# Kernel optimization log

Measured on AMD Instinct MI355X. Metric: run time of the kernel, lower is better.

Reference implementation:

```python
import jax, jax.numpy as jnp
import numpy as np

N_NODES = 100000
N_EDGES = 500000
IN_DIM, HID, N_CLS = 128, 512, 40


def gcn_conv(x, W, b, src, dst, num_nodes):
    # PyG GCNConv: h = x W; add self-loops; norm = d^-1/2[src] * d^-1/2[dst];
    # out[dst] += norm * h[src]; out += bias
    h = x @ W  # [N, out_dim]
    ones = jnp.ones(src.shape[0], dtype=x.dtype)
    deg = jax.ops.segment_sum(ones, dst, num_segments=num_nodes)  # in-degree incl self-loops
    dinv = jnp.where(deg > 0, jax.lax.rsqrt(deg), 0.0)
    norm = dinv[src] * dinv[dst]  # [E]
    msgs = h[src] * norm[:, None]  # [E, out_dim] gather + scale
    out = jax.ops.segment_sum(msgs, dst, num_segments=num_nodes)
    return out + b


def setup_inputs() -> dict:
    key = jax.random.key(0)
    k1, k2, k3, k4, k5, k6 = jax.random.split(key, 6)
    x = jax.random.normal(k1, (N_NODES, IN_DIM), dtype=jnp.float32)
    edge_index = jax.random.randint(k2, (2, N_EDGES), 0, N_NODES, dtype=jnp.int32)
    # Glorot-ish params
    W1 = jax.random.normal(k3, (IN_DIM, HID), dtype=jnp.float32) * (1.0 / np.sqrt(IN_DIM))
    b1 = jnp.zeros((HID,), dtype=jnp.float32)
    W2 = jax.random.normal(k4, (HID, N_CLS), dtype=jnp.float32) * (1.0 / np.sqrt(HID))
    b2 = jnp.zeros((N_CLS,), dtype=jnp.float32)
    return {"x": x, "edge_index": edge_index, "W1": W1, "b1": b1, "W2": W2, "b2": b2}


def reference(x, edge_index, W1, b1, W2, b2):
    n = x.shape[0]
    # add self-loops once, shared by both conv layers
    loop = jnp.arange(n, dtype=edge_index.dtype)
    src = jnp.concatenate([edge_index[0], loop])
    dst = jnp.concatenate([edge_index[1], loop])
    h = gcn_conv(x, W1, b1, src, dst, n)
    h = jax.nn.relu(h)
    # dropout is identity in eval mode (reference computed in eval)
    h = gcn_conv(h, W2, b2, src, dst, n)
    return jax.nn.log_softmax(h, axis=1)
```

## Files before the change

kernel.cpp:

```cpp
#include <hip/hip_runtime.h>
#include <cstdint>
#include <cstddef>

#define N_NODES 100000
#define N_EDGES 500000
#define IN_DIM  128
#define HID     512
#define N_CLS   40
#define N_SBLK  ((N_NODES + 255) / 256)
#define N_CNTB  ((N_EDGES + 255) / 256)
#define N_XBFB  12500
#define N_PREPB 352

typedef short bf16x8 __attribute__((ext_vector_type(8)));
typedef float f32x4 __attribute__((ext_vector_type(4)));

__device__ inline unsigned short f2bf(float f) {
  unsigned u = __float_as_uint(f);
  u = u + 0x7fffu + ((u >> 16) & 1u);
  return (unsigned short)(u >> 16);
}
__device__ inline float blo(unsigned u) { return __uint_as_float(u << 16); }
__device__ inline float bhi(unsigned u) { return __uint_as_float(u & 0xffff0000u); }
__device__ inline float bf2f(unsigned short s) { return __uint_as_float((unsigned)s << 16); }

__global__ __launch_bounds__(256) void k_zero(int* __restrict__ cnt) {
  int i = blockIdx.x * 256 + threadIdx.x;
  if (i < N_NODES) cnt[i] = 0;
}

__global__ __launch_bounds__(256) void k_count_xbf(const int* __restrict__ dst, int* __restrict__ cnt,
                                                   const float* __restrict__ x, uint2* __restrict__ xb2) {
  int b = blockIdx.x;
  if (b < N_CNTB) {
    int e = b * 256 + threadIdx.x;
    if (e < N_EDGES) atomicAdd(&cnt[dst[e]], 1);
  } else {
    int t = (b - N_CNTB) * 256 + threadIdx.x;
    float4 v = ((const float4*)x)[t];
    uint2 o;
    o.x = (unsigned)f2bf(v.x) | ((unsigned)f2bf(v.y) << 16);
    o.y = (unsigned)f2bf(v.z) | ((unsigned)f2bf(v.w) << 16);
    xb2[t] = o;
  }
}

__global__ __launch_bounds__(256) void k_scan1(const int* __restrict__ cnt, int* __restrict__ lofs,
                                               int* __restrict__ blksum, float* __restrict__ dinv) {
  __shared__ int s[256];
  int i = blockIdx.x * 256 + threadIdx.x;
  int v = (i < N_NODES) ? cnt[i] : 0;
  s[threadIdx.x] = v;
  __syncthreads();
  #pragma unroll
  for (int off = 1; off < 256; off <<= 1) {
    int t = (threadIdx.x >= off) ? s[threadIdx.x - off] : 0;
    __syncthreads();
    s[threadIdx.x] += t;
    __syncthreads();
  }
  if (i < N_NODES) {
    lofs[i] = s[threadIdx.x] - v;
    dinv[i] = rsqrtf((float)(v + 1));
  }
  if (threadIdx.x == 255) blksum[blockIdx.x] = s[255];
}

__global__ __launch_bounds__(512) void k_scan2(const int* __restrict__ blksum, int* __restrict__ blkbase) {
  __shared__ int s[512];
  int t = threadIdx.x;
  int v = (t < N_SBLK) ? blksum[t] : 0;
  s[t] = v;
  __syncthreads();
  #pragma unroll
  for (int off = 1; off < 512; off <<= 1) {
    int u = (t >= off) ? s[t - off] : 0;
    __syncthreads();
    s[t] += u;
    __syncthreads();
  }
  if (t < N_SBLK) blkbase[t] = s[t] - v;
}

__global__ __launch_bounds__(256) void k_scan3_prep(const int* __restrict__ lofs, const int* __restrict__ blkbase,
                                                    int* __restrict__ offsets, int* __restrict__ cursor,
                                                    const float* __restrict__ W1, const float* __restrict__ W2,
                                                    unsigned short* __restrict__ W1F, unsigned short* __restrict__ W2F) {
  int b = blockIdx.x;
  if (b < N_SBLK) {
    int i = b * 256 + threadIdx.x;
    if (b == 0 && threadIdx.x == 0) offsets[N_NODES] = N_EDGES;
    if (i >= N_NODES) return;
    int base = blkbase[b] + lofs[i];
    offsets[i] = base;
    cursor[i]  = base;
  } else {
    int t = (b - N_SBLK) * 256 + threadIdx.x;
    if (t < 65536) {
      int j = t & 7, lane = (t >> 3) & 63, rest = t >> 9;
      int s = rest & 3, c = rest >> 2;
      int k = s * 32 + (lane >> 4) * 8 + j;
      int n = c * 16 + (lane & 15);
      W1F[t] = f2bf(W1[k * HID + n]);
    } else {
      int u = t - 65536;
      int j = u & 7, lane = (u >> 3) & 63, rest = u >> 9;
      int ct = rest % 3, gk = rest / 3;
      int k = gk * 32 + (lane >> 4) * 8 + j;
      int col = ct * 16 + (lane & 15);
      W2F[u] = (col < N_CLS) ? f2bf(W2[k * N_CLS + col]) : (unsigned short)0;
    }
  }
}

__global__ __launch_bounds__(256) void k_fill(const int* __restrict__ src, const int* __restrict__ dst,
                                              const float* __restrict__ dinv,
                                              int* __restrict__ cursor, int2* __restrict__ epair) {
  int e = blockIdx.x * 256 + threadIdx.x;
  if (e >= N_EDGES) return;
  int s = src[e], d = dst[e];
  int pos = atomicAdd(&cursor[d], 1);
  float nrm = dinv[s] * dinv[d];
  epair[pos] = make_int2(s, __float_as_int(nrm));
}

__global__ __launch_bounds__(256) void k_gather1(const uint4* __restrict__ xb4, const int2* __restrict__ ep,
                                                 const int* __restrict__ offsets,
                                                 const float* __restrict__ dinv, uint4* __restrict__ z1b4) {
  int d = blockIdx.x * 4 + (threadIdx.x >> 6);
  if (d >= N_NODES) return;
  int lane = threadIdx.x & 63, q = lane >> 4, l16 = lane & 15;
  int start = offsets[d], end = offsets[d + 1];

  float a0 = 0.f, a1 = 0.f, a2 = 0.f, a3 = 0.f, a4 = 0.f, a5 = 0.f, a6 = 0.f, a7 = 0.f;
  if (q == 0) {
    float dd = dinv[d], sl = dd * dd;
    uint4 u = xb4[(size_t)d * 16 + l16];
    a0 = sl * blo(u.x); a1 = sl * bhi(u.x); a2 = sl * blo(u.y); a3 = sl * bhi(u.y);
    a4 = sl * blo(u.z); a5 = sl * bhi(u.z); a6 = sl * blo(u.w); a7 = sl * bhi(u.w);
  }

  int i = start + q;
  for (; i + 4 < end; i += 8) {
    int2 p0 = ep[i], p1 = ep[i + 4];
    uint4 r0 = xb4[(size_t)p0.x * 16 + l16];
    uint4 r1 = xb4[(size_t)p1.x * 16 + l16];
    float n0 = __int_as_float(p0.y), n1 = __int_as_float(p1.y);
    a0 += n0 * blo(r0.x); a1 += n0 * bhi(r0.x); a2 += n0 * blo(r0.y); a3 += n0 * bhi(r0.y);
    a4 += n0 * blo(r0.z); a5 += n0 * bhi(r0.z); a6 += n0 * blo(r0.w); a7 += n0 * bhi(r0.w);
    a0 += n1 * blo(r1.x); a1 += n1 * bhi(r1.x); a2 += n1 * blo(r1.y); a3 += n1 * bhi(r1.y);
    a4 += n1 * blo(r1.z); a5 += n1 * bhi(r1.z); a6 += n1 * blo(r1.w); a7 += n1 * bhi(r1.w);
  }
  for (; i < end; i += 4) {
    int2 p = ep[i];
    uint4 r = xb4[(size_t)p.x * 16 + l16];
    float n = __int_as_float(p.y);
    a0 += n * blo(r.x); a1 += n * bhi(r.x); a2 += n * blo(r.y); a3 += n * bhi(r.y);
    a4 += n * blo(r.z); a5 += n * bhi(r.z); a6 += n * blo(r.w); a7 += n * bhi(r.w);
  }

  a0 += __shfl_xor(a0, 16, 64); a0 += __shfl_xor(a0, 32, 64);
  a1 += __shfl_xor(a1, 16, 64); a1 += __shfl_xor(a1, 32, 64);
  a2 += __shfl_xor(a2, 16, 64); a2 += __shfl_xor(a2, 32, 64);
  a3 += __shfl_xor(a3, 16, 64); a3 += __shfl_xor(a3, 32, 64);
  a4 += __shfl_xor(a4, 16, 64); a4 += __shfl_xor(a4, 32, 64);
  a5 += __shfl_xor(a5, 16, 64); a5 += __shfl_xor(a5, 32, 64);
  a6 += __shfl_xor(a6, 16, 64); a6 += __shfl_xor(a6, 32, 64);
  a7 += __shfl_xor(a7, 16, 64); a7 += __shfl_xor(a7, 32, 64);
  if (q == 0) {
    uint4 o;
    o.x = (unsigned)f2bf(a0) | ((unsigned)f2bf(a1) << 16);
    o.y = (unsigned)f2bf(a2) | ((unsigned)f2bf(a3) << 16);
    o.z = (unsigned)f2bf(a4) | ((unsigned)f2bf(a5) << 16);
    o.w = (unsigned)f2bf(a6) | ((unsigned)f2bf(a7) << 16);
    z1b4[(size_t)d * 16 + l16] = o;
  }
}

#define HS_STRIDE 56
__global__ __launch_bounds__(256) void k_fused_mfma(const unsigned short* __restrict__ z1b,
                                                    const unsigned short* __restrict__ W1F,
                                                    const float* __restrict__ b1,
                                                    const unsigned short* __restrict__ W2F,
                                                    unsigned short* __restrict__ Pb) {
  __shared__ unsigned short Hs[4][64 * HS_STRIDE];
  const int tid  = threadIdx.x;
  const int w    = tid >> 6, lane = tid & 63;
  const int c16  = lane & 15, quad = lane >> 4;
  const int mbase = blockIdx.x * 256 + w * 64;

  bf16x8 afrag[4][4];
  #pragma unroll
  for (int t = 0; t < 4; ++t) {
    int mrow = mbase + t * 16 + c16;
    int meff = (mrow < N_NODES) ? mrow : 0;
    const bf16x8* arow = (const bf16x8*)(z1b + (size_t)meff * IN_DIM + quad * 8);
    afrag[t][0] = arow[0];
    afrag[t][1] = arow[4];
    afrag[t][2] = arow[8];
    afrag[t][3] = arow[12];
  }

  f32x4 pacc[4][3];
  #pragma unroll
  for (int t = 0; t < 4; ++t)
    #pragma unroll
    for (int ct = 0; ct < 3; ++ct) pacc[t][ct] = (f32x4){0.f, 0.f, 0.f, 0.f};

  const bf16x8* w1f = (const bf16x8*)W1F;
  const bf16x8* w2f = (const bf16x8*)W2F;
  unsigned short* hs = Hs[w];

  for (int g = 0; g < 16; ++g) {
    #pragma unroll
    for (int nt = 0; nt < 2; ++nt) {
      int c = g * 2 + nt;
      bf16x8 bp0 = w1f[(c * 4 + 0) * 64 + lane];
      bf16x8 bp1 = w1f[(c * 4 + 1) * 64 + lane];
      bf16x8 bp2 = w1f[(c * 4 + 2) * 64 + lane];
      bf16x8 bp3 = w1f[(c * 4 + 3) * 64 + lane];
      f32x4 h[4];
      #pragma unroll
      for (int t = 0; t < 4; ++t) h[t] = (f32x4){0.f, 0.f, 0.f, 0.f};
      #pragma unroll
      for (int t = 0; t < 4; ++t) h[t] = __builtin_amdgcn_mfma_f32_16x16x32_bf16(afrag[t][0], bp0, h[t], 0, 0, 0);
      #pragma unroll
      for (int t = 0; t < 4; ++t) h[t] = __builtin_amdgcn_mfma_f32_16x16x32_bf16(afrag[t][1], bp1, h[t], 0, 0, 0);
      #pragma unroll
      for (int t = 0; t < 4; ++t) h[t] = __builtin_amdgcn_mfma_f32_16x16x32_bf16(afrag[t][2], bp2, h[t], 0, 0, 0);
      #pragma unroll
      for (int t = 0; t < 4; ++t) h[t] = __builtin_amdgcn_mfma_f32_16x16x32_bf16(afrag[t][3], bp3, h[t], 0, 0, 0);
      float bias = b1[c * 16 + c16];
      #pragma unroll
      for (int t = 0; t < 4; ++t)
        #pragma unroll
        for (int r = 0; r < 4; ++r)
          hs[(t * 16 + quad * 4 + r) * HS_STRIDE + nt * 16 + c16] = f2bf(fmaxf(h[t][r] + bias, 0.f));
    }
    bf16x8 hf[4];
    #pragma unroll
    for (int t = 0; t < 4; ++t)
      hf[t] = *(const bf16x8*)(hs + (t * 16 + c16) * HS_STRIDE + quad * 8);
    #pragma unroll
    for (int ct = 0; ct < 3; ++ct) {
      bf16x8 bf = w2f[(g * 3 + ct) * 64 + lane];
      #pragma unroll
      for (int t = 0; t < 4; ++t)
        pacc[t][ct] = __builtin_amdgcn_mfma_f32_16x16x32_bf16(hf[t], bf, pacc[t][ct], 0, 0, 0);
    }
  }

  #pragma unroll
  for (int t = 0; t < 4; ++t) {
    int mrow0 = mbase + t * 16 + quad * 4;
    #pragma unroll
    for (int ct = 0; ct < 3; ++ct) {
      int col = ct * 16 + c16;
      if (col < N_CLS) {
        #pragma unroll
        for (int r = 0; r < 4; ++r) {
          int m = mrow0 + r;
          if (m < N_NODES) Pb[(size_t)m * N_CLS + col] = f2bf(pacc[t][ct][r]);
        }
      }
    }
  }
}

__global__ __launch_bounds__(256) void k_gather2_lsm(const unsigned* __restrict__ Pu,
                                                     const int2* __restrict__ ep,
                                                     const int* __restrict__ offsets,
                                                     const float* __restrict__ dinv, const float* __restrict__ b2,
                                                     float* __restrict__ out) {
  int lane = threadIdx.x & 63, h = lane >> 5, l32 = lane & 31;
  int d = blockIdx.x * 8 + (threadIdx.x >> 6) * 2 + h;
  bool act = l32 < 20;
  int lc = act ? l32 : 0;
  int start = offsets[d], end = offsets[d + 1];
  float dd = dinv[d];

  float x0, y0, x1 = 0.f, y1 = 0.f, x2 = 0.f, y2 = 0.f, x3 = 0.f, y3 = 0.f;
  {
    unsigned u = Pu[(size_t)d * 20 + lc];
    float sl = dd * dd;
    x0 = sl * blo(u); y0 = sl * bhi(u);
  }
  int i = start;
  for (; i + 3 < end; i += 4) {
    int2 p0 = ep[i], p1 = ep[i + 1], p2 = ep[i + 2], p3 = ep[i + 3];
    unsigned u0 = Pu[(size_t)p0.x * 20 + lc];
    unsigned u1 = Pu[(size_t)p1.x * 20 + lc];
    unsigned u2 = Pu[(size_t)p2.x * 20 + lc];
    unsigned u3 = Pu[(size_t)p3.x * 20 + lc];
    float n0 = __int_as_float(p0.y), n1 = __int_as_float(p1.y);
    float n2 = __int_as_float(p2.y), n3 = __int_as_float(p3.y);
    x0 += n0 * blo(u0); y0 += n0 * bhi(u0);
    x1 += n1 * blo(u1); y1 += n1 * bhi(u1);
    x2 += n2 * blo(u2); y2 += n2 * bhi(u2);
    x3 += n3 * blo(u3); y3 += n3 * bhi(u3);
  }
  for (; i < end; ++i) {
    int2 p = ep[i];
    unsigned u = Pu[(size_t)p.x * 20 + lc];
    float n = __int_as_float(p.y);
    x0 += n * blo(u); y0 += n * bhi(u);
  }

  float v0, v1;
  if (act) {
    float2 bb = *(const float2*)(b2 + 2 * l32);
    v0 = x0 + x1 + x2 + x3 + bb.x;
    v1 = y0 + y1 + y2 + y3 + bb.y;
  } else {
    v0 = v1 = -1e30f;
  }
  float m = fmaxf(v0, v1);
  #pragma unroll
  for (int off = 16; off > 0; off >>= 1) m = fmaxf(m, __shfl_xor(m, off, 64));
  float e = act ? (expf(v0 - m) + expf(v1 - m)) : 0.f;
  float s = e;
  #pragma unroll
  for (int off = 16; off > 0; off >>= 1) s += __shfl_xor(s, off, 64);
  float lse = m + logf(s);
  if (act) {
    float2 o = make_float2(v0 - lse, v1 - lse);
    *(float2*)(out + (size_t)d * N_CLS + 2 * l32) = o;
  }
}

extern "C" void kernel_launch(void* const* d_in, const int* in_sizes, int n_in,
                              void* d_out, int out_size, void* d_ws, size_t ws_size,
                              hipStream_t stream) {
  const float* x  = (const float*)d_in[0];
  const int*   ei = (const int*)d_in[1];
  const int*  src = ei;
  const int*  dst = ei + N_EDGES;
  const float* W1 = (const float*)d_in[2];
  const float* b1 = (const float*)d_in[3];
  const float* W2 = (const float*)d_in[4];
  const float* b2 = (const float*)d_in[5];
  float* out = (float*)d_out;

  float* dinv    = (float*)d_ws;
  int*   cnt     = (int*)(dinv + 131072);
  int*   offsets = cnt + 131072;
  int*   cursor  = offsets + 131072;
  int*   lofs    = cursor + 131072;
  int*   blksum  = lofs + 131072;
  int*   blkbase = blksum + 512;
  int2*  epair   = (int2*)(blkbase + 512);
  uint2* xb2     = (uint2*)(epair + 524288);
  unsigned short* Pb = (unsigned short*)xb2;
  unsigned short* z1b = (unsigned short*)(xb2 + 3200000);
  unsigned short* W1F = z1b + (size_t)N_NODES * IN_DIM;
  unsigned short* W2F = W1F + HID * IN_DIM;

  k_zero <<<(N_NODES + 255) / 256, 256, 0, stream>>>(cnt);
  k_count_xbf<<<N_CNTB + N_XBFB, 256, 0, stream>>>(dst, cnt, x, xb2);
  k_scan1<<<N_SBLK, 256, 0, stream>>>(cnt, lofs, blksum, dinv);
  k_scan2<<<1, 512, 0, stream>>>(blksum, blkbase);
  k_scan3_prep<<<N_SBLK + N_PREPB, 256, 0, stream>>>(lofs, blkbase, offsets, cursor, W1, W2, W1F, W2F);
  k_fill <<<N_CNTB, 256, 0, stream>>>(src, dst, dinv, cursor, epair);
  k_gather1<<<(N_NODES + 3) / 4, 256, 0, stream>>>((const uint4*)xb2, epair, offsets, dinv, (uint4*)z1b);
  k_fused_mfma<<<(N_NODES + 255) / 256, 256, 0, stream>>>(z1b, W1F, b1, W2F, Pb);
  k_gather2_lsm<<<N_NODES / 8, 256, 0, stream>>>((const unsigned*)Pb, epair, offsets, dinv, b2, out);
}
```

Before: 249.2 us.

## Fuse three-pass scan into decoupled look-back scan and remap gather lanes

Replaces the three scan kernels with a single kernel that uses a decoupled look-back (per-block flag/aggregate) prefix scan, cutting two launches and the intermediate arrays. The look-back relies on blocks making forward progress, since a block spins on its predecessor. It also remaps gather1 so each half-wave handles one node with 4 bf16 per lane and four independent accumulators, replacing the quarter-wave split and cross-lane shuffle reduction. Gather2 now packs four nodes per wave with 4 classes per lane.

Measured after the change: 247.4 us. Within noise of the previous version (-0.7%).

```diff
diff --git a/kernel.cpp b/kernel.cpp
--- a/kernel.cpp
+++ b/kernel.cpp
@@ -22,11 +22,11 @@
 }
 __device__ inline float blo(unsigned u) { return __uint_as_float(u << 16); }
 __device__ inline float bhi(unsigned u) { return __uint_as_float(u & 0xffff0000u); }
-__device__ inline float bf2f(unsigned short s) { return __uint_as_float((unsigned)s << 16); }
-
-__global__ __launch_bounds__(256) void k_zero(int* __restrict__ cnt) {
+
+__global__ __launch_bounds__(256) void k_zero(int* __restrict__ cnt, unsigned* __restrict__ flags) {
   int i = blockIdx.x * 256 + threadIdx.x;
   if (i < N_NODES) cnt[i] = 0;
+  if (i < 512) flags[i] = 0;
 }
 
 __global__ __launch_bounds__(256) void k_count_xbf(const int* __restrict__ dst, int* __restrict__ cnt,
@@ -45,61 +45,61 @@
   }
 }
 
-__global__ __launch_bounds__(256) void k_scan1(const int* __restrict__ cnt, int* __restrict__ lofs,
-                                               int* __restrict__ blksum, float* __restrict__ dinv) {
-  __shared__ int s[256];
-  int i = blockIdx.x * 256 + threadIdx.x;
-  int v = (i < N_NODES) ? cnt[i] : 0;
-  s[threadIdx.x] = v;
-  __syncthreads();
-  #pragma unroll
-  for (int off = 1; off < 256; off <<= 1) {
-    int t = (threadIdx.x >= off) ? s[threadIdx.x - off] : 0;
-    __syncthreads();
-    s[threadIdx.x] += t;
-    __syncthreads();
-  }
-  if (i < N_NODES) {
-    lofs[i] = s[threadIdx.x] - v;
-    dinv[i] = rsqrtf((float)(v + 1));
-  }
-  if (threadIdx.x == 255) blksum[blockIdx.x] = s[255];
-}
-
-__global__ __launch_bounds__(512) void k_scan2(const int* __restrict__ blksum, int* __restrict__ blkbase) {
-  __shared__ int s[512];
-  int t = threadIdx.x;
-  int v = (t < N_SBLK) ? blksum[t] : 0;
-  s[t] = v;
-  __syncthreads();
-  #pragma unroll
-  for (int off = 1; off < 512; off <<= 1) {
-    int u = (t >= off) ? s[t - off] : 0;
-    __syncthreads();
-    s[t] += u;
-    __syncthreads();
-  }
-  if (t < N_SBLK) blkbase[t] = s[t] - v;
-}
-
-__global__ __launch_bounds__(256) void k_scan3_prep(const int* __restrict__ lofs, const int* __restrict__ blkbase,
-                                                    int* __restrict__ offsets, int* __restrict__ cursor,
-                                                    const float* __restrict__ W1, const float* __restrict__ W2,
-                                                    unsigned short* __restrict__ W1F, unsigned short* __restrict__ W2F) {
+__global__ __launch_bounds__(256) void k_scan_prep(const int* __restrict__ cnt, unsigned* __restrict__ flags,
+                                                   int* __restrict__ offsets, int* __restrict__ cursor,
+                                                   float* __restrict__ dinv,
+                                                   const float* __restrict__ W1, const float* __restrict__ W2,
+                                                   unsigned short* __restrict__ W1F, unsigned short* __restrict__ W2F) {
   int b = blockIdx.x;
   if (b < N_SBLK) {
+    __shared__ int s[256];
+    __shared__ int base_sh;
     int i = b * 256 + threadIdx.x;
+    int v = (i < N_NODES) ? cnt[i] : 0;
+    s[threadIdx.x] = v;
+    __syncthreads();
+    #pragma unroll
+    for (int off = 1; off < 256; off <<= 1) {
+      int t = (threadIdx.x >= off) ? s[threadIdx.x - off] : 0;
+      __syncthreads();
+      s[threadIdx.x] += t;
+      __syncthreads();
+    }
+    int incl = s[threadIdx.x];
+    if (threadIdx.x == 0) {
+      int total = s[255];
+      if (b == 0) {
+        atomicExch(&flags[0], (2u << 30) | (unsigned)total);
+        base_sh = 0;
+      } else {
+        atomicExch(&flags[b], (1u << 30) | (unsigned)total);
+        int base = 0, pred = b - 1;
+        while (true) {
+          unsigned f;
+          do { f = atomicAdd(&flags[pred], 0u); } while ((f >> 30) == 0u);
+          base += (int)(f & 0x3fffffffu);
+          if ((f >> 30) == 2u) break;
+          --pred;
+        }
+        atomicExch(&flags[b], (2u << 30) | (unsigned)(base + (unsigned)total));
+        base_sh = base;
+      }
+    }
+    __syncthreads();
+    int gbase = base_sh;
+    if (i < N_NODES) {
+      int excl = gbase + incl - v;
+      offsets[i] = excl;
+      cursor[i]  = excl;
+      dinv[i]    = rsqrtf((float)(v + 1));
+    }
     if (b == 0 && threadIdx.x == 0) offsets[N_NODES] = N_EDGES;
-    if (i >= N_NODES) return;
-    int base = blkbase[b] + lofs[i];
-    offsets[i] = base;
-    cursor[i]  = base;
   } else {
     int t = (b - N_SBLK) * 256 + threadIdx.x;
     if (t < 65536) {
       int j = t & 7, lane = (t >> 3) & 63, rest = t >> 9;
-      int s = rest & 3, c = rest >> 2;
-      int k = s * 32 + (lane >> 4) * 8 + j;
+      int s2 = rest & 3, c = rest >> 2;
+      int k = s2 * 32 + (lane >> 4) * 8 + j;
       int n = c * 16 + (lane & 15);
       W1F[t] = f2bf(W1[k * HID + n]);
     } else {
@@ -124,57 +124,47 @@
   epair[pos] = make_int2(s, __float_as_int(nrm));
 }
 
-__global__ __launch_bounds__(256) void k_gather1(const uint4* __restrict__ xb4, const int2* __restrict__ ep,
+__global__ __launch_bounds__(256) void k_gather1(const uint2* __restrict__ xb, const int2* __restrict__ ep,
                                                  const int* __restrict__ offsets,
-                                                 const float* __restrict__ dinv, uint4* __restrict__ z1b4) {
-  int d = blockIdx.x * 4 + (threadIdx.x >> 6);
-  if (d >= N_NODES) return;
-  int lane = threadIdx.x & 63, q = lane >> 4, l16 = lane & 15;
+                                                 const float* __restrict__ dinv, uint2* __restrict__ z1) {
+  int lane = threadIdx.x & 63, h = lane >> 5, l = lane & 31;
+  int d = blockIdx.x * 8 + (threadIdx.x >> 6) * 2 + h;
   int start = offsets[d], end = offsets[d + 1];
-
-  float a0 = 0.f, a1 = 0.f, a2 = 0.f, a3 = 0.f, a4 = 0.f, a5 = 0.f, a6 = 0.f, a7 = 0.f;
-  if (q == 0) {
-    float dd = dinv[d], sl = dd * dd;
-    uint4 u = xb4[(size_t)d * 16 + l16];
-    a0 = sl * blo(u.x); a1 = sl * bhi(u.x); a2 = sl * blo(u.y); a3 = sl * bhi(u.y);
-    a4 = sl * blo(u.z); a5 = sl * bhi(u.z); a6 = sl * blo(u.w); a7 = sl * bhi(u.w);
-  }
-
-  int i = start + q;
-  for (; i + 4 < end; i += 8) {
-    int2 p0 = ep[i], p1 = ep[i + 4];
-    uint4 r0 = xb4[(size_t)p0.x * 16 + l16];
-    uint4 r1 = xb4[(size_t)p1.x * 16 + l16];
-    float n0 = __int_as_float(p0.y), n1 = __int_as_float(p1.y);
+  float dd = dinv[d], sl = dd * dd;
+  uint2 su = xb[(size_t)d * 32 + l];
+  float a0 = sl * blo(su.x), a1 = sl * bhi(su.x), a2 = sl * blo(su.y), a3 = sl * bhi(su.y);
+  float p0a = 0.f, p1a = 0.f, p2a = 0.f, p3a = 0.f;
+  float q0a = 0.f, q1a = 0.f, q2a = 0.f, q3a = 0.f;
+  float r0a = 0.f, r1a = 0.f, r2a = 0.f, r3a = 0.f;
+
+  int i = start;
+  for (; i + 3 < end; i += 4) {
+    int2 e0 = ep[i], e1 = ep[i + 1], e2 = ep[i + 2], e3 = ep[i + 3];
+    uint2 r0 = xb[(size_t)e0.x * 32 + l];
+    uint2 r1 = xb[(size_t)e1.x * 32 + l];
+    uint2 r2 = xb[(size_t)e2.x * 32 + l];
+    uint2 r3 = xb[(size_t)e3.x * 32 + l];
+    float n0 = __int_as_float(e0.y), n1 = __int_as_float(e1.y);
+    float n2 = __int_as_float(e2.y), n3 = __int_as_float(e3.y);
+    a0  += n0 * blo(r0.x); a1  += n0 * bhi(r0.x); a2  += n0 * blo(r0.y); a3  += n0 * bhi(r0.y);
+    p0a += n1 * blo(r1.x); p1a += n1 * bhi(r1.x); p2a += n1 * blo(r1.y); p3a += n1 * bhi(r1.y);
+    q0a += n2 * blo(r2.x); q1a += n2 * bhi(r2.x); q2a += n2 * blo(r2.y); q3a += n2 * bhi(r2.y);
+    r0a += n3 * blo(r3.x); r1a += n3 * bhi(r3.x); r2a += n3 * blo(r3.y); r3a += n3 * bhi(r3.y);
+  }
+  for (; i < end; ++i) {
+    int2 e0 = ep[i];
+    uint2 r0 = xb[(size_t)e0.x * 32 + l];
+    float n0 = __int_as_float(e0.y);
     a0 += n0 * blo(r0.x); a1 += n0 * bhi(r0.x); a2 += n0 * blo(r0.y); a3 += n0 * bhi(r0.y);
-    a4 += n0 * blo(r0.z); a5 += n0 * bhi(r0.z); a6 += n0 * blo(r0.w); a7 += n0 * bhi(r0.w);
-    a0 += n1 * blo(r1.x); a1 += n1 * bhi(r1.x); a2 += n1 * blo(r1.y); a3 += n1 * bhi(r1.y);
-    a4 += n1 * blo(r1.z); a5 += n1 * bhi(r1.z); a6 += n1 * blo(r1.w); a7 += n1 * bhi(r1.w);
-  }
-  for (; i < end; i += 4) {
-    int2 p = ep[i];
-    uint4 r = xb4[(size_t)p.x * 16 + l16];
-    float n = __int_as_float(p.y);
-    a0 += n * blo(r.x); a1 += n * bhi(r.x); a2 += n * blo(r.y); a3 += n * bhi(r.y);
-    a4 += n * blo(r.z); a5 += n * bhi(r.z); a6 += n * blo(r.w); a7 += n * bhi(r.w);
-  }
-
-  a0 += __shfl_xor(a0, 16, 64); a0 += __shfl_xor(a0, 32, 64);
-  a1 += __shfl_xor(a1, 16, 64); a1 += __shfl_xor(a1, 32, 64);
-  a2 += __shfl_xor(a2, 16, 64); a2 += __shfl_xor(a2, 32, 64);
-  a3 += __shfl_xor(a3, 16, 64); a3 += __shfl_xor(a3, 32, 64);
-  a4 += __shfl_xor(a4, 16, 64); a4 += __shfl_xor(a4, 32, 64);
-  a5 += __shfl_xor(a5, 16, 64); a5 += __shfl_xor(a5, 32, 64);
-  a6 += __shfl_xor(a6, 16, 64); a6 += __shfl_xor(a6, 32, 64);
-  a7 += __shfl_xor(a7, 16, 64); a7 += __shfl_xor(a7, 32, 64);
-  if (q == 0) {
-    uint4 o;
-    o.x = (unsigned)f2bf(a0) | ((unsigned)f2bf(a1) << 16);
-    o.y = (unsigned)f2bf(a2) | ((unsigned)f2bf(a3) << 16);
-    o.z = (unsigned)f2bf(a4) | ((unsigned)f2bf(a5) << 16);
-    o.w = (unsigned)f2bf(a6) | ((unsigned)f2bf(a7) << 16);
-    z1b4[(size_t)d * 16 + l16] = o;
-  }
+  }
+  a0 += p0a + q0a + r0a;
+  a1 += p1a + q1a + r1a;
+  a2 += p2a + q2a + r2a;
+  a3 += p3a + q3a + r3a;
+  uint2 o;
+  o.x = (unsigned)f2bf(a0) | ((unsigned)f2bf(a1) << 16);
+  o.y = (unsigned)f2bf(a2) | ((unsigned)f2bf(a3) << 16);
+  z1[(size_t)d * 32 + l] = o;
 }
 
 #define HS_STRIDE 56
@@ -267,64 +257,66 @@
   }
 }
 
-__global__ __launch_bounds__(256) void k_gather2_lsm(const unsigned* __restrict__ Pu,
+__global__ __launch_bounds__(256) void k_gather2_lsm(const uint2* __restrict__ Pu2,
                                                      const int2* __restrict__ ep,
                                                      const int* __restrict__ offsets,
                                                      const float* __restrict__ dinv, const float* __restrict__ b2,
                                                      float* __restrict__ out) {
-  int lane = threadIdx.x & 63, h = lane >> 5, l32 = lane & 31;
-  int d = blockIdx.x * 8 + (threadIdx.x >> 6) * 2 + h;
-  bool act = l32 < 20;
-  int lc = act ? l32 : 0;
+  int lane = threadIdx.x & 63, q = lane >> 4, l = lane & 15;
+  int d = blockIdx.x * 16 + (threadIdx.x >> 6) * 4 + q;
+  bool act = l < 10;
+  int lc = act ? l : 0;
   int start = offsets[d], end = offsets[d + 1];
-  float dd = dinv[d];
-
-  float x0, y0, x1 = 0.f, y1 = 0.f, x2 = 0.f, y2 = 0.f, x3 = 0.f, y3 = 0.f;
-  {
-    unsigned u = Pu[(size_t)d * 20 + lc];
-    float sl = dd * dd;
-    x0 = sl * blo(u); y0 = sl * bhi(u);
-  }
+  float dd = dinv[d], sl = dd * dd;
+
+  uint2 su = Pu2[(size_t)d * 10 + lc];
+  float a0 = sl * blo(su.x), a1 = sl * bhi(su.x), a2 = sl * blo(su.y), a3 = sl * bhi(su.y);
+  float p0a = 0.f, p1a = 0.f, p2a = 0.f, p3a = 0.f;
+  float q0a = 0.f, q1a = 0.f, q2a = 0.f, q3a = 0.f;
+  float r0a = 0.f, r1a = 0.f, r2a = 0.f, r3a = 0.f;
+
   int i = start;
   for (; i + 3 < end; i += 4) {
-    int2 p0 = ep[i], p1 = ep[i + 1], p2 = ep[i + 2], p3 = ep[i + 3];
-    unsigned u0 = Pu[(size_t)p0.x * 20 + lc];
-    unsigned u1 = Pu[(size_t)p1.x * 20 + lc];
-    unsigned u2 = Pu[(size_t)p2.x * 20 + lc];
-    unsigned u3 = Pu[(size_t)p3.x * 20 + lc];
-    float n0 = __int_as_float(p0.y), n1 = __int_as_float(p1.y);
-    float n2 = __int_as_float(p2.y), n3 = __int_as_float(p3.y);
-    x0 += n0 * blo(u0); y0 += n0 * bhi(u0);
-    x1 += n1 * blo(u1); y1 += n1 * bhi(u1);
-    x2 += n2 * blo(u2); y2 += n2 * bhi(u2);
-    x3 += n3 * blo(u3); y3 += n3 * bhi(u3);
+    int2 e0 = ep[i], e1 = ep[i + 1], e2 = ep[i + 2], e3 = ep[i + 3];
+    uint2 u0 = Pu2[(size_t)e0.x * 10 + lc];
+    uint2 u1 = Pu2[(size_t)e1.x * 10 + lc];
+    uint2 u2 = Pu2[(size_t)e2.x * 10 + lc];
+    uint2 u3 = Pu2[(size_t)e3.x * 10 + lc];
+    float n0 = __int_as_float(e0.y), n1 = __int_as_float(e1.y);
+    float n2 = __int_as_float(e2.y), n3 = __int_as_float(e3.y);
+    a0  += n0 * blo(u0.x); a1  += n0 * bhi(u0.x); a2  += n0 * blo(u0.y); a3  += n0 * bhi(u0.y);
+    p0a += n1 * blo(u1.x); p1a += n1 * bhi(u1.x); p2a += n1 * blo(u1.y); p3a += n1 * bhi(u1.y);
+    q0a += n2 * blo(u2.x); q1a += n2 * bhi(u2.x); q2a += n2 * blo(u2.y); q3a += n2 * bhi(u2.y);
+    r0a += n3 * blo(u3.x); r1a += n3 * bhi(u3.x); r2a += n3 * blo(u3.y); r3a += n3 * bhi(u3.y);
   }
   for (; i < end; ++i) {
-    int2 p = ep[i];
-    unsigned u = Pu[(size_t)p.x * 20 + lc];
-    float n = __int_as_float(p.y);
-    x0 += n * blo(u); y0 += n * bhi(u);
-  }
-
-  float v0, v1;
+    int2 e0 = ep[i];
+    uint2 u0 = Pu2[(size_t)e0.x * 10 + lc];
+    float n0 = __int_as_float(e0.y);
+    a0 += n0 * blo(u0.x); a1 += n0 * bhi(u0.x); a2 += n0 * blo(u0.y); a3 += n0 * bhi(u0.y);
+  }
+
+  float v0, v1, v2, v3;
   if (act) {
-    float2 bb = *(const float2*)(b2 + 2 * l32);
-    v0 = x0 + x1 + x2 + x3 + bb.x;
-    v1 = y0 + y1 + y2 + y3 + bb.y;
+    float4 bb = ((const float4*)b2)[l];
+    v0 = a0 + p0a + q0a + r0a + bb.x;
+    v1 = a1 + p1a + q1a + r1a + bb.y;
+    v2 = a2 + p2a + q2a + r2a + bb.z;
+    v3 = a3 + p3a + q3a + r3a + bb.w;
   } else {
-    v0 = v1 = -1e30f;
-  }
-  float m = fmaxf(v0, v1);
-  #pragma unroll
-  for (int off = 16; off > 0; off >>= 1) m = fmaxf(m, __shfl_xor(m, off, 64));
-  float e = act ? (expf(v0 - m) + expf(v1 - m)) : 0.f;
+    v0 = v1 = v2 = v3 = -1e30f;
+  }
+  float m = fmaxf(fmaxf(v0, v1), fmaxf(v2, v3));
+  #pragma unroll
+  for (int off = 8; off > 0; off >>= 1) m = fmaxf(m, __shfl_xor(m, off, 64));
+  float e = act ? (expf(v0 - m) + expf(v1 - m) + expf(v2 - m) + expf(v3 - m)) : 0.f;
   float s = e;
   #pragma unroll
-  for (int off = 16; off > 0; off >>= 1) s += __shfl_xor(s, off, 64);
+  for (int off = 8; off > 0; off >>= 1) s += __shfl_xor(s, off, 64);
   float lse = m + logf(s);
   if (act) {
-    float2 o = make_float2(v0 - lse, v1 - lse);
-    *(float2*)(out + (size_t)d * N_CLS + 2 * l32) = o;
+    float4 o = make_float4(v0 - lse, v1 - lse, v2 - lse, v3 - lse);
+    ((float4*)(out + (size_t)d * N_CLS))[l] = o;
   }
 }
 
@@ -345,23 +337,19 @@
   int*   cnt     = (int*)(dinv + 131072);
   int*   offsets = cnt + 131072;
   int*   cursor  = offsets + 131072;
-  int*   lofs    = cursor + 131072;
-  int*   blksum  = lofs + 131072;
-  int*   blkbase = blksum + 512;
-  int2*  epair   = (int2*)(blkbase + 512);
+  unsigned* flags = (unsigned*)(cursor + 131072);
+  int2*  epair   = (int2*)(flags + 1024);
   uint2* xb2     = (uint2*)(epair + 524288);
   unsigned short* Pb = (unsigned short*)xb2;
   unsigned short* z1b = (unsigned short*)(xb2 + 3200000);
   unsigned short* W1F = z1b + (size_t)N_NODES * IN_DIM;
   unsigned short* W2F = W1F + HID * IN_DIM;
 
-  k_zero <<<(N_NODES + 255) / 256, 256, 0, stream>>>(cnt);
+  k_zero <<<(N_NODES + 255) / 256, 256, 0, stream>>>(cnt, flags);
   k_count_xbf<<<N_CNTB + N_XBFB, 256, 0, stream>>>(dst, cnt, x, xb2);
-  k_scan1<<<N_SBLK, 256, 0, stream>>>(cnt, lofs, blksum, dinv);
-  k_scan2<<<1, 512, 0, stream>>>(blksum, blkbase);
-  k_scan3_prep<<<N_SBLK + N_PREPB, 256, 0, stream>>>(lofs, blkbase, offsets, cursor, W1, W2, W1F, W2F);
+  k_scan_prep<<<N_SBLK + N_PREPB, 256, 0, stream>>>(cnt, flags, offsets, cursor, dinv, W1, W2, W1F, W2F);
   k_fill <<<N_CNTB, 256, 0, stream>>>(src, dst, dinv, cursor, epair);
-  k_gather1<<<(N_NODES + 3) / 4, 256, 0, stream>>>((const uint4*)xb2, epair, offsets, dinv, (uint4*)z1b);
+  k_gather1<<<N_NODES / 8, 256, 0, stream>>>(xb2, epair, offsets, dinv, (uint2*)z1b);
   k_fused_mfma<<<(N_NODES + 255) / 256, 256, 0, stream>>>(z1b, W1F, b1, W2F, Pb);
-  k_gather2_lsm<<<N_NODES / 8, 256, 0, stream>>>((const unsigned*)Pb, epair, offsets, dinv, b2, out);
-}
+  k_gather2_lsm<<<N_NODES / 16, 256, 0, stream>>>((const uint2*)Pb, epair, offsets, dinv, b2, out);
+}
```
